# Optimization experiments

Hardware: AMD Instinct MI355X
Metric: run time of the kernel (lower is better)

## Reference

```python
import jax, jax.numpy as jnp
import numpy as np

B, N, DIM, HEADS = 4, 2048, 512, 8
LN_EPS = 1e-5


def setup_inputs() -> dict:
    key = jax.random.key(0)
    ks = jax.random.split(key, 16)
    w = lambda k: jax.random.normal(k, (DIM, DIM), jnp.float32) * 0.02
    bv = lambda k: jax.random.normal(k, (DIM,), jnp.float32) * 0.02
    return {
        'x': jax.random.normal(ks[0], (B, N, DIM), jnp.float32),
        'y': jax.random.normal(ks[1], (B, N, DIM), jnp.float32),
        'Wq': w(ks[2]), 'bq': bv(ks[3]),
        'Wk': w(ks[4]), 'bk': bv(ks[5]),
        'Wvr': w(ks[6]), 'bvr': bv(ks[7]),
        'Wvd': w(ks[8]), 'bvd': bv(ks[9]),
        'g_r': jnp.ones((DIM,), jnp.float32), 'b_r': jnp.zeros((DIM,), jnp.float32),
        'g_d': jnp.ones((DIM,), jnp.float32), 'b_d': jnp.zeros((DIM,), jnp.float32),
        'Wpr': w(ks[10]), 'bpr': bv(ks[11]),
        'Wpd': w(ks[12]), 'bpd': bv(ks[13]),
        'num_heads': HEADS,
    }


def _ln(t, g, b):
    mu = jnp.mean(t, axis=-1, keepdims=True)
    var = jnp.mean(jnp.square(t - mu), axis=-1, keepdims=True)
    return (t - mu) * jax.lax.rsqrt(var + LN_EPS) * g + b


def reference(x, y, Wq, bq, Wk, bk, Wvr, bvr, Wvd, bvd,
              g_r, b_r, g_d, b_d, Wpr, bpr, Wpd, bpd, num_heads):
    Bn, Nn, C = x.shape
    D = C // num_heads
    xn = _ln(x, g_r, b_r)   # norm_r(x)
    yn = _ln(y, g_d, b_d)   # norm_d(y)

    def heads(t, W, b):  # Linear then split heads -> (B, H, N, D)
        return (t @ W.T + b).reshape(Bn, Nn, num_heads, D).transpose(0, 2, 1, 3)

    q_r = heads(yn, Wq, bq)    # query from depth-normed y
    v_r = heads(xn, Wvr, bvr)
    k_d = heads(xn, Wk, bk)
    v_d = heads(xn, Wvd, bvd)

    scale = D ** -0.5
    attn = jnp.einsum('bhnd,bhmd->bhnm', q_r, k_d) * scale  # shared QK^T
    attn_r = jax.nn.softmax(attn, axis=-1)                  # row-wise
    attn_d = jax.nn.softmax(attn.transpose(0, 1, 3, 2), axis=-1)  # col-wise (transposed)

    out_r = jnp.einsum('bhnm,bhmd->bhnd', attn_r, v_r)
    out_r = out_r.transpose(0, 2, 1, 3).reshape(Bn, Nn, C) @ Wpr.T + bpr

    o_d = jnp.einsum('bhnm,bhmd->bhnd', attn_d, v_d)
    o_d = o_d.transpose(0, 2, 1, 3).reshape(Bn, Nn, C)
    # Faithful to source quirk: extra transpose(1,2)+reshape scrambles layout.
    o_d = o_d.transpose(0, 2, 1).reshape(Bn, Nn, C)
    out_d = o_d @ Wpd.T + bpd
    return out_r, out_d
```

## Files before the change

kernel.cpp:

```cpp
#include <hip/hip_runtime.h>
#include <hip/hip_bf16.h>

typedef __hip_bfloat16 bf16;
typedef __attribute__((ext_vector_type(8))) short short8;
typedef __attribute__((ext_vector_type(4))) short short4v;
typedef __attribute__((ext_vector_type(4))) float floatx4;

static constexpr int B = 4;
static constexpr int N = 2048;
static constexpr int C = 512;
static constexpr int H = 8;
static constexpr int D = 64;

#define QK_SCALE 0.18033688011112042f

__device__ int g_flags[18];

__device__ __forceinline__ float u2f(unsigned short u) {
    return __uint_as_float(((unsigned int)u) << 16);
}
__device__ __forceinline__ unsigned short f2bf(float f) {
    unsigned int u = __float_as_uint(f);
    return (unsigned short)((u + 0x7FFFu + ((u >> 16) & 1u)) >> 16);
}
__device__ __forceinline__ float ldin(const void* p, size_t i, int f) {
    if (f == 2) return 0.0f;
    return f ? ((const float*)p)[i] : u2f(((const unsigned short*)p)[i]);
}

__device__ __forceinline__ void gl_lds16(const unsigned short* g, unsigned short* l) {
    __builtin_amdgcn_global_load_lds(
        (const __attribute__((address_space(1))) unsigned int*)g,
        (__attribute__((address_space(3))) unsigned int*)l,
        16, 0, 0);
}

struct Ptrs { const void* p[18]; };

__global__ void detect_kernel(Ptrs ptrs) {
    int t = blockIdx.x;
    int lane = threadIdx.x;
    unsigned int v = ((const unsigned int*)ptrs.p[t])[lane];
    unsigned int e = (v >> 7) & 0xFF;
    unsigned long long mp = __ballot(e >= 96 && e <= 144);
    unsigned long long mz = __ballot(v != 0u);
    if (lane == 0)
        g_flags[t] = (mz == 0ull) ? 2 : ((__popcll(mp) >= 32) ? 0 : 1);
}

__global__ __launch_bounds__(256) void convert_w(Ptrs ptrs, bf16* dst) {
    int wsel = blockIdx.y;
    int wi = wsel < 4 ? 2 + 2 * wsel : 14 + 2 * (wsel - 4);
    int f = g_flags[wi];
    const void* src = ptrs.p[wi];
    unsigned short* out = (unsigned short*)dst + (size_t)wsel * 262144;
    int base = (blockIdx.x * 256 + threadIdx.x) * 16;
    if (f == 1) {
        const float4* s = (const float4*)((const float*)src + base);
        float4 f0 = s[0], f1 = s[1], f2 = s[2], f3 = s[3];
        uint4 o0, o1;
        o0.x = f2bf(f0.x) | ((unsigned int)f2bf(f0.y) << 16);
        o0.y = f2bf(f0.z) | ((unsigned int)f2bf(f0.w) << 16);
        o0.z = f2bf(f1.x) | ((unsigned int)f2bf(f1.y) << 16);
        o0.w = f2bf(f1.z) | ((unsigned int)f2bf(f1.w) << 16);
        o1.x = f2bf(f2.x) | ((unsigned int)f2bf(f2.y) << 16);
        o1.y = f2bf(f2.z) | ((unsigned int)f2bf(f2.w) << 16);
        o1.z = f2bf(f3.x) | ((unsigned int)f2bf(f3.y) << 16);
        o1.w = f2bf(f3.z) | ((unsigned int)f2bf(f3.w) << 16);
        *(uint4*)(out + base) = o0;
        *(uint4*)(out + base + 8) = o1;
    } else if (f == 0) {
        const uint4* s = (const uint4*)((const unsigned short*)src + base);
        uint4 a = s[0], b2 = s[1];
        *(uint4*)(out + base) = a;
        *(uint4*)(out + base + 8) = b2;
    } else {
        uint4 z = {0, 0, 0, 0};
        *(uint4*)(out + base) = z;
        *(uint4*)(out + base + 8) = z;
    }
}

__global__ __launch_bounds__(256) void ln_kernel(
    const void* __restrict__ x, const void* __restrict__ y,
    const void* __restrict__ g_r, const void* __restrict__ b_r,
    const void* __restrict__ g_d, const void* __restrict__ b_d,
    bf16* __restrict__ xn, bf16* __restrict__ yn)
{
    __shared__ float ls[4], lq[4];
    __shared__ float mu_s, rs_s;

    int row = blockIdx.x;
    bool isY = row >= B * N;
    int r = isY ? row - B * N : row;
    const void* src = isY ? y : x;
    int sf = isY ? g_flags[1] : g_flags[0];
    const void* g  = isY ? g_d : g_r;
    int gf = isY ? g_flags[12] : g_flags[10];
    const void* bb = isY ? b_d : b_r;
    int bflag = isY ? g_flags[13] : g_flags[11];
    bf16* dst = (isY ? yn : xn) + (size_t)r * C;
    size_t base = (size_t)r * C;

    int tid = threadIdx.x;
    float v0 = ldin(src, base + tid, sf);
    float v1 = ldin(src, base + tid + 256, sf);
    float s = v0 + v1, sq = v0 * v0 + v1 * v1;
    #pragma unroll
    for (int off = 32; off > 0; off >>= 1) {
        s  += __shfl_down(s, off);
        sq += __shfl_down(sq, off);
    }
    int wid = tid >> 6, lane = tid & 63;
    if (lane == 0) { ls[wid] = s; lq[wid] = sq; }
    __syncthreads();
    if (tid == 0) {
        float S = ls[0] + ls[1] + ls[2] + ls[3];
        float Q = lq[0] + lq[1] + lq[2] + lq[3];
        float mu = S * (1.0f / C);
        float var = Q * (1.0f / C) - mu * mu;
        mu_s = mu; rs_s = rsqrtf(var + 1e-5f);
    }
    __syncthreads();
    float mu = mu_s, rs = rs_s;
    dst[tid]       = __float2bfloat16((v0 - mu) * rs * ldin(g, tid, gf)       + ldin(bb, tid, bflag));
    dst[tid + 256] = __float2bfloat16((v1 - mu) * rs * ldin(g, tid + 256, gf) + ldin(bb, tid + 256, bflag));
}

__device__ __forceinline__ void gemm_core(
    const bf16* __restrict__ A, const bf16* __restrict__ W,
    const void* __restrict__ bias, int bflag, void* __restrict__ Cout,
    int omode, float oscale)
{
    __shared__ __align__(16) unsigned short As[3][128 * 32];
    __shared__ __align__(16) unsigned short Ws[3][64 * 32];

    int tid = threadIdx.x;
    int n0 = blockIdx.x * 64;
    int m0 = blockIdx.y * 128;

    int wave = tid >> 6, lane = tid & 63;
    int wm = (wave >> 1) * 64, wn = (wave & 1) * 32;
    int quad = lane >> 4, mr = lane & 15;

    floatx4 acc[4][2] = {};

    int c0 = tid, c1 = 256 + tid;
    const unsigned short* Ag0 = (const unsigned short*)A + (size_t)(m0 + (c0 >> 2)) * 512 + (c0 & 3) * 8;
    const unsigned short* Ag1 = (const unsigned short*)A + (size_t)(m0 + (c1 >> 2)) * 512 + (c1 & 3) * 8;
    const unsigned short* Wg0 = (const unsigned short*)W + (size_t)(n0 + (c0 >> 2)) * 512 + (c0 & 3) * 8;

    auto STAGE = [&](int kt, int bsel) {
        int ko = kt * 32;
        gl_lds16(Ag0 + ko, &As[bsel][c0 * 8]);
        gl_lds16(Ag1 + ko, &As[bsel][c1 * 8]);
        gl_lds16(Wg0 + ko, &Ws[bsel][c0 * 8]);
    };

    auto GBODY = [&](int bsel, int kt) {
        if (kt < 14) {
            STAGE(kt + 2, bsel == 0 ? 2 : bsel - 1);
            asm volatile("s_waitcnt vmcnt(6)" ::: "memory");
        } else if (kt == 14) {
            asm volatile("s_waitcnt vmcnt(3)" ::: "memory");
        } else {
            asm volatile("s_waitcnt vmcnt(0)" ::: "memory");
        }
        __builtin_amdgcn_s_barrier();
        __builtin_amdgcn_sched_barrier(0);

        short8 af[4], bfr[2];
        #pragma unroll
        for (int i = 0; i < 4; ++i)
            af[i] = *(const short8*)&As[bsel][(wm + i * 16 + mr) * 32 + quad * 8];
        #pragma unroll
        for (int j = 0; j < 2; ++j)
            bfr[j] = *(const short8*)&Ws[bsel][(wn + j * 16 + mr) * 32 + quad * 8];
        #pragma unroll
        for (int i = 0; i < 4; ++i)
            #pragma unroll
            for (int j = 0; j < 2; ++j)
                acc[i][j] = __builtin_amdgcn_mfma_f32_16x16x32_bf16(
                    af[i], bfr[j], acc[i][j], 0, 0, 0);

        __builtin_amdgcn_sched_barrier(0);
        __builtin_amdgcn_s_barrier();
    };

    STAGE(0, 0);
    STAGE(1, 1);
    for (int g = 0; g < 5; ++g) {
        int kt = g * 3;
        GBODY(0, kt);
        GBODY(1, kt + 1);
        GBODY(2, kt + 2);
    }
    GBODY(0, 15);

    float bv[2];
    #pragma unroll
    for (int j = 0; j < 2; ++j)
        bv[j] = ldin(bias, n0 + wn + j * 16 + mr, bflag);
    #pragma unroll
    for (int i = 0; i < 4; ++i) {
        #pragma unroll
        for (int j = 0; j < 2; ++j) {
            int o = n0 + wn + j * 16 + mr;
            #pragma unroll
            for (int reg = 0; reg < 4; ++reg) {
                int r = m0 + wm + i * 16 + quad * 4 + reg;
                float val = (acc[i][j][reg] + bv[j]) * oscale;
                if (omode == 0) {
                    ((bf16*)Cout)[(size_t)r * 512 + o] = __float2bfloat16(val);
                } else if (omode == 1) {
                    ((float*)Cout)[(size_t)r * 512 + o] = val;
                } else {
                    int batch = r >> 11, nn = r & 2047;
                    ((bf16*)Cout)[((size_t)(batch * 512 + o)) * 2048 + nn] =
                        __float2bfloat16(val);
                }
            }
        }
    }
}

__global__ __launch_bounds__(256) void gemm_stage(
    const bf16* __restrict__ xn, const bf16* __restrict__ yn,
    const bf16* __restrict__ wts, Ptrs ptrs,
    bf16* __restrict__ q, bf16* __restrict__ k,
    bf16* __restrict__ vrT, bf16* __restrict__ vdT)
{
    int z = blockIdx.z;
    const bf16* A = (z == 0) ? yn : xn;
    const bf16* W = wts + (size_t)z * 262144;
    int bi = 3 + 2 * z;
    void* Cout = (z == 0) ? (void*)q : (z == 1) ? (void*)k
               : (z == 2) ? (void*)vrT : (void*)vdT;
    int omode = (z < 2) ? 0 : 2;
    float oscale = (z == 0) ? QK_SCALE : 1.0f;
    gemm_core(A, W, ptrs.p[bi], g_flags[bi], Cout, omode, oscale);
}

__global__ __launch_bounds__(256) void gemm_out(
    const bf16* __restrict__ Or, const bf16* __restrict__ Ad,
    const bf16* __restrict__ wts, Ptrs ptrs,
    float* __restrict__ out0, float* __restrict__ out1)
{
    int z = blockIdx.z;
    const bf16* A = z ? Ad : Or;
    const bf16* W = wts + (size_t)(4 + z) * 262144;
    int bi = 15 + 2 * z;
    gemm_core(A, W, ptrs.p[bi], g_flags[bi], z ? (void*)out1 : (void*)out0, 1, 1.0f);
}

__global__ __launch_bounds__(256) void flash_mfma(
    const bf16* __restrict__ qm, const bf16* __restrict__ km,
    const bf16* __restrict__ vrT, const bf16* __restrict__ vdT,
    bf16* __restrict__ Or, bf16* __restrict__ Ad)
{
    __shared__ __align__(16) unsigned short Ks[2][64 * 64];
    __shared__ __align__(16) unsigned short Vs[2][64 * 64];

    int phys = blockIdx.x + 32 * blockIdx.y + 256 * blockIdx.z;
    int s = phys >> 3;
    int qblk = s & 31;
    int gidx = (phys & 7) + ((s >> 5) << 3);
    int pass = gidx >> 5;
    int b = (gidx >> 3) & 3;
    int h = gidx & 7;

    const bf16* Q  = pass ? km : qm;
    const bf16* K  = pass ? qm : km;
    const bf16* Vt = pass ? vdT : vrT;
    bf16* Out = pass ? Ad : Or;

    int tid = threadIdx.x;
    int wave = tid >> 6, lane = tid & 63;
    int quad = lane >> 4, mr = lane & 15;
    int m8 = mr & 7;
    int qw = qblk * 64 + wave * 16;

    const unsigned short* Qb = (const unsigned short*)Q + ((size_t)(b * N + qw + mr)) * C + h * D;
    short8 qf0 = *(const short8*)(Qb + quad * 8);
    short8 qf1 = *(const short8*)(Qb + 32 + quad * 8);

    floatx4 Oacc[4] = {};
    floatx4 lacc = {};

    short4v ones;
    {
        union { unsigned int u[2]; short4v s4; } cv;
        cv.u[0] = 0x3F803F80u; cv.u[1] = 0x3F803F80u;
        ones = cv.s4;
    }

    int c0 = tid, c1 = 256 + tid;
    int r0 = c0 >> 3, cs0 = c0 & 7;
    int r1 = c1 >> 3, cs1 = c1 & 7;
    const unsigned short* Kb  = (const unsigned short*)K + ((size_t)b * N) * C + h * D;
    const unsigned short* Vtb = (const unsigned short*)Vt + ((size_t)(b * 512 + h * 64)) * 2048;
    const unsigned short* sk0 = Kb + (size_t)r0 * C + ((cs0 ^ (r0 & 7)) << 3);
    const unsigned short* sk1 = Kb + (size_t)r1 * C + ((cs1 ^ (r1 & 7)) << 3);
    const unsigned short* sv0 = Vtb + (size_t)r0 * 2048 + ((cs0 ^ (r0 & 7)) << 3);
    const unsigned short* sv1 = Vtb + (size_t)r1 * 2048 + ((cs1 ^ (r1 & 7)) << 3);

    auto STAGE = [&](int bsel) {
        gl_lds16(sk0, &Ks[bsel][c0 * 8]);
        gl_lds16(sk1, &Ks[bsel][c1 * 8]);
        gl_lds16(sv0, &Vs[bsel][c0 * 8]);
        gl_lds16(sv1, &Vs[bsel][c1 * 8]);
        sk0 += 64 * C; sk1 += 64 * C; sv0 += 64; sv1 += 64;
    };

    int skc0 = (quad ^ m8) << 3;
    int skc1 = ((quad + 4) ^ m8) << 3;
    int vq = quad >> 1, vlo = (quad & 1) * 4;

    auto BODY = [&](int cur, bool last) {
        if (!last) {
            STAGE(cur ^ 1);
            asm volatile("s_waitcnt vmcnt(4)" ::: "memory");
        } else {
            asm volatile("s_waitcnt vmcnt(0)" ::: "memory");
        }
        __builtin_amdgcn_s_barrier();
        __builtin_amdgcn_sched_barrier(0);

        floatx4 tac[4] = {};
        __builtin_amdgcn_s_setprio(1);
        #pragma unroll
        for (int t = 0; t < 4; ++t) {
            const unsigned short* kr = &Ks[cur][(t * 16 + mr) * 64];
            short8 kf0 = *(const short8*)(kr + skc0);
            short8 kf1 = *(const short8*)(kr + skc1);
            tac[t] = __builtin_amdgcn_mfma_f32_16x16x32_bf16(kf0, qf0, tac[t], 0, 0, 0);
            tac[t] = __builtin_amdgcn_mfma_f32_16x16x32_bf16(kf1, qf1, tac[t], 0, 0, 0);
        }
        __builtin_amdgcn_s_setprio(0);

        short4v pa[4];
        #pragma unroll
        for (int t = 0; t < 4; ++t) {
            float p0, p1, p2, p3;
            asm("v_exp_f32 %0, %1" : "=v"(p0) : "v"(tac[t][0]));
            asm("v_exp_f32 %0, %1" : "=v"(p1) : "v"(tac[t][1]));
            asm("v_exp_f32 %0, %1" : "=v"(p2) : "v"(tac[t][2]));
            asm("v_exp_f32 %0, %1" : "=v"(p3) : "v"(tac[t][3]));
            unsigned int u0, u1;
            asm("v_cvt_pk_bf16_f32 %0, %1, %2" : "=v"(u0) : "v"(p0), "v"(p1));
            asm("v_cvt_pk_bf16_f32 %0, %1, %2" : "=v"(u1) : "v"(p2), "v"(p3));
            union { unsigned int u[2]; short4v s4; } cv;
            cv.u[0] = u0; cv.u[1] = u1;
            pa[t] = cv.s4;
        }

        __builtin_amdgcn_s_setprio(1);
        #pragma unroll
        for (int t = 0; t < 4; ++t) {
            int vslot = (((2 * t + vq) ^ m8) << 3) + vlo;
            #pragma unroll
            for (int j = 0; j < 4; ++j) {
                short4v vb = *(const short4v*)&Vs[cur][(j * 16 + mr) * 64 + vslot];
                Oacc[j] = __builtin_amdgcn_mfma_f32_16x16x16bf16_1k(
                    pa[t], vb, Oacc[j], 0, 0, 0);
            }
            lacc = __builtin_amdgcn_mfma_f32_16x16x16bf16_1k(pa[t], ones, lacc, 0, 0, 0);
        }
        __builtin_amdgcn_s_setprio(0);

        __builtin_amdgcn_sched_barrier(0);
        __builtin_amdgcn_s_barrier();
    };

    STAGE(0);
    for (int kt2 = 0; kt2 < 15; ++kt2) {
        BODY(0, false);
        BODY(1, false);
    }
    BODY(0, false);
    BODY(1, true);

    float inv[4];
    #pragma unroll
    for (int r = 0; r < 4; ++r)
        inv[r] = 1.0f / lacc[r];

    if (pass == 0) {
        #pragma unroll
        for (int t = 0; t < 4; ++t)
            #pragma unroll
            for (int r = 0; r < 4; ++r) {
                int n = qw + quad * 4 + r;
                Out[((size_t)(b * N + n)) * C + h * D + t * 16 + mr] =
                    __float2bfloat16(Oacc[t][r] * inv[r]);
            }
    } else {
        size_t bbase = (size_t)b * N * C;
        #pragma unroll
        for (int t = 0; t < 4; ++t)
            #pragma unroll
            for (int r = 0; r < 4; ++r) {
                int n = qw + quad * 4 + r;
                int c = h * D + t * 16 + mr;
                Out[bbase + (size_t)(c * 4 + (n >> 9)) * 512 + (n & 511)] =
                    __float2bfloat16(Oacc[t][r] * inv[r]);
            }
    }
}

extern "C" void kernel_launch(void* const* d_in, const int* in_sizes, int n_in,
                              void* d_out, int out_size, void* d_ws, size_t ws_size,
                              hipStream_t stream)
{
    const void* x   = d_in[0];
    const void* y   = d_in[1];
    const void* g_r = d_in[10];
    const void* b_r = d_in[11];
    const void* g_d = d_in[12];
    const void* b_d = d_in[13];

    Ptrs ptrs;
    for (int i = 0; i < 18; ++i) ptrs.p[i] = d_in[i];

    const size_t SL = (size_t)B * N * C;

    char* wsb = (char*)d_ws;
    bf16* q   = (bf16*)wsb;
    bf16* k   = (bf16*)(wsb + 8ull * 1024 * 1024);
    bf16* vrT = (bf16*)(wsb + 16ull * 1024 * 1024);
    bf16* vdT = (bf16*)(wsb + 24ull * 1024 * 1024);
    bf16* xn  = (bf16*)(wsb + 32ull * 1024 * 1024);
    bf16* yn  = (bf16*)(wsb + 40ull * 1024 * 1024);
    bf16* wts = (bf16*)(wsb + 48ull * 1024 * 1024);
    bf16* Or = xn;
    bf16* Ad = yn;

    float* out0 = (float*)d_out;
    float* out1 = (float*)d_out + SL;

    detect_kernel<<<18, 64, 0, stream>>>(ptrs);
    convert_w<<<dim3(64, 6), 256, 0, stream>>>(ptrs, wts);
    ln_kernel<<<2 * B * N, 256, 0, stream>>>(x, y, g_r, b_r, g_d, b_d, xn, yn);

    gemm_stage<<<dim3(8, 64, 4), 256, 0, stream>>>(xn, yn, wts, ptrs, q, k, vrT, vdT);

    dim3 fg(32, 8, 8);
    flash_mfma<<<fg, 256, 0, stream>>>(q, k, vrT, vdT, Or, Ad);

    gemm_out<<<dim3(8, 64, 2), 256, 0, stream>>>(Or, Ad, wts, ptrs, out0, out1);
}
```

Before: 303.2 us.

## Fuse K/Vr/Vd projections, vectorize LayerNorm per-wave, trim flash barriers

LayerNorm now handles one row per wave with 8-element vector loads and a pure shuffle reduction, removing the LDS round trips and block-level syncs. The K, Vr and Vd projections, which share the input xn, are fused into one GEMM kernel. Each A tile is loaded once and reused against three weight tiles, so xn is read from memory once instead of three times. The Q projection moves to its own kernel. The flash attention loop drops the trailing barrier and places a single barrier before staging, which cuts synchronisation per iteration. The fused GEMM holds three times the accumulators and uses more LDS, so occupancy may fall.

```diff
diff --git a/kernel.cpp b/kernel.cpp
--- a/kernel.cpp
+++ b/kernel.cpp
@@ -26,6 +26,22 @@
 __device__ __forceinline__ float ldin(const void* p, size_t i, int f) {
     if (f == 2) return 0.0f;
     return f ? ((const float*)p)[i] : u2f(((const unsigned short*)p)[i]);
+}
+
+__device__ __forceinline__ void ld8(const void* p, size_t idx, int f, float* o) {
+    if (f == 1) {
+        const float4* q = (const float4*)((const float*)p + idx);
+        float4 a = q[0], b2 = q[1];
+        o[0] = a.x; o[1] = a.y; o[2] = a.z; o[3] = a.w;
+        o[4] = b2.x; o[5] = b2.y; o[6] = b2.z; o[7] = b2.w;
+    } else if (f == 0) {
+        short8 s8 = *(const short8*)((const unsigned short*)p + idx);
+        #pragma unroll
+        for (int i = 0; i < 8; ++i) o[i] = u2f((unsigned short)s8[i]);
+    } else {
+        #pragma unroll
+        for (int i = 0; i < 8; ++i) o[i] = 0.0f;
+    }
 }
 
 __device__ __forceinline__ void gl_lds16(const unsigned short* g, unsigned short* l) {
@@ -87,10 +103,9 @@
     const void* __restrict__ g_d, const void* __restrict__ b_d,
     bf16* __restrict__ xn, bf16* __restrict__ yn)
 {
-    __shared__ float ls[4], lq[4];
-    __shared__ float mu_s, rs_s;
-
-    int row = blockIdx.x;
+    int tid = threadIdx.x;
+    int wid = tid >> 6, lane = tid & 63;
+    int row = blockIdx.x * 4 + wid;
     bool isY = row >= B * N;
     int r = isY ? row - B * N : row;
     const void* src = isY ? y : x;
@@ -100,31 +115,32 @@
     const void* bb = isY ? b_d : b_r;
     int bflag = isY ? g_flags[13] : g_flags[11];
     bf16* dst = (isY ? yn : xn) + (size_t)r * C;
-    size_t base = (size_t)r * C;
-
-    int tid = threadIdx.x;
-    float v0 = ldin(src, base + tid, sf);
-    float v1 = ldin(src, base + tid + 256, sf);
-    float s = v0 + v1, sq = v0 * v0 + v1 * v1;
-    #pragma unroll
-    for (int off = 32; off > 0; off >>= 1) {
-        s  += __shfl_down(s, off);
-        sq += __shfl_down(sq, off);
-    }
-    int wid = tid >> 6, lane = tid & 63;
-    if (lane == 0) { ls[wid] = s; lq[wid] = sq; }
-    __syncthreads();
-    if (tid == 0) {
-        float S = ls[0] + ls[1] + ls[2] + ls[3];
-        float Q = lq[0] + lq[1] + lq[2] + lq[3];
-        float mu = S * (1.0f / C);
-        float var = Q * (1.0f / C) - mu * mu;
-        mu_s = mu; rs_s = rsqrtf(var + 1e-5f);
-    }
-    __syncthreads();
-    float mu = mu_s, rs = rs_s;
-    dst[tid]       = __float2bfloat16((v0 - mu) * rs * ldin(g, tid, gf)       + ldin(bb, tid, bflag));
-    dst[tid + 256] = __float2bfloat16((v1 - mu) * rs * ldin(g, tid + 256, gf) + ldin(bb, tid + 256, bflag));
+
+    int col = lane * 8;
+    float v[8];
+    ld8(src, (size_t)r * C + col, sf, v);
+
+    float s = 0.f, sq = 0.f;
+    #pragma unroll
+    for (int i = 0; i < 8; ++i) { s += v[i]; sq += v[i] * v[i]; }
+    #pragma unroll
+    for (int off = 1; off < 64; off <<= 1) {
+        s  += __shfl_xor(s, off);
+        sq += __shfl_xor(sq, off);
+    }
+    float mu = s * (1.0f / C);
+    float var = sq * (1.0f / C) - mu * mu;
+    float rs = rsqrtf(var + 1e-5f);
+
+    float gv[8], bv[8];
+    ld8(g, col, gf, gv);
+    ld8(bb, col, bflag, bv);
+
+    union { unsigned short us[8]; short8 s8; } o;
+    #pragma unroll
+    for (int i = 0; i < 8; ++i)
+        o.us[i] = f2bf((v[i] - mu) * rs * gv[i] + bv[i]);
+    *(short8*)(dst + col) = o.s8;
 }
 
 __device__ __forceinline__ void gemm_core(
@@ -224,21 +240,11 @@
     }
 }
 
-__global__ __launch_bounds__(256) void gemm_stage(
-    const bf16* __restrict__ xn, const bf16* __restrict__ yn,
-    const bf16* __restrict__ wts, Ptrs ptrs,
-    bf16* __restrict__ q, bf16* __restrict__ k,
-    bf16* __restrict__ vrT, bf16* __restrict__ vdT)
-{
-    int z = blockIdx.z;
-    const bf16* A = (z == 0) ? yn : xn;
-    const bf16* W = wts + (size_t)z * 262144;
-    int bi = 3 + 2 * z;
-    void* Cout = (z == 0) ? (void*)q : (z == 1) ? (void*)k
-               : (z == 2) ? (void*)vrT : (void*)vdT;
-    int omode = (z < 2) ? 0 : 2;
-    float oscale = (z == 0) ? QK_SCALE : 1.0f;
-    gemm_core(A, W, ptrs.p[bi], g_flags[bi], Cout, omode, oscale);
+__global__ __launch_bounds__(256) void gemm_q(
+    const bf16* __restrict__ yn, const bf16* __restrict__ wts, Ptrs ptrs,
+    bf16* __restrict__ q)
+{
+    gemm_core(yn, wts, ptrs.p[3], g_flags[3], (void*)q, 0, QK_SCALE);
 }
 
 __global__ __launch_bounds__(256) void gemm_out(
@@ -251,6 +257,115 @@
     const bf16* W = wts + (size_t)(4 + z) * 262144;
     int bi = 15 + 2 * z;
     gemm_core(A, W, ptrs.p[bi], g_flags[bi], z ? (void*)out1 : (void*)out0, 1, 1.0f);
+}
+
+__global__ __launch_bounds__(256) void gemm_fused3(
+    const bf16* __restrict__ xn, const bf16* __restrict__ wts, Ptrs ptrs,
+    bf16* __restrict__ k, bf16* __restrict__ vrT, bf16* __restrict__ vdT)
+{
+    __shared__ __align__(16) unsigned short As[3][128 * 32];
+    __shared__ __align__(16) unsigned short Ws[3][3][64 * 32];
+
+    int tid = threadIdx.x;
+    int n0 = blockIdx.x * 64;
+    int m0 = blockIdx.y * 128;
+
+    int wave = tid >> 6, lane = tid & 63;
+    int wm = (wave >> 1) * 64, wn = (wave & 1) * 32;
+    int quad = lane >> 4, mr = lane & 15;
+
+    floatx4 acc[3][4][2] = {};
+
+    int c0 = tid, c1 = 256 + tid;
+    const unsigned short* Ag0 = (const unsigned short*)xn + (size_t)(m0 + (c0 >> 2)) * 512 + (c0 & 3) * 8;
+    const unsigned short* Ag1 = (const unsigned short*)xn + (size_t)(m0 + (c1 >> 2)) * 512 + (c1 & 3) * 8;
+    const unsigned short* Wg[3];
+    #pragma unroll
+    for (int z = 0; z < 3; ++z)
+        Wg[z] = (const unsigned short*)wts + (size_t)(1 + z) * 262144
+              + (size_t)(n0 + (c0 >> 2)) * 512 + (c0 & 3) * 8;
+
+    auto STAGE = [&](int kt, int bsel) {
+        int ko = kt * 32;
+        gl_lds16(Ag0 + ko, &As[bsel][c0 * 8]);
+        gl_lds16(Ag1 + ko, &As[bsel][c1 * 8]);
+        #pragma unroll
+        for (int z = 0; z < 3; ++z)
+            gl_lds16(Wg[z] + ko, &Ws[bsel][z][c0 * 8]);
+    };
+
+    auto GBODY = [&](int bsel, int kt) {
+        if (kt < 14) {
+            STAGE(kt + 2, bsel == 0 ? 2 : bsel - 1);
+            asm volatile("s_waitcnt vmcnt(10)" ::: "memory");
+        } else if (kt == 14) {
+            asm volatile("s_waitcnt vmcnt(5)" ::: "memory");
+        } else {
+            asm volatile("s_waitcnt vmcnt(0)" ::: "memory");
+        }
+        __builtin_amdgcn_s_barrier();
+        __builtin_amdgcn_sched_barrier(0);
+
+        short8 af[4];
+        #pragma unroll
+        for (int i = 0; i < 4; ++i)
+            af[i] = *(const short8*)&As[bsel][(wm + i * 16 + mr) * 32 + quad * 8];
+        #pragma unroll
+        for (int z = 0; z < 3; ++z) {
+            short8 bfr[2];
+            #pragma unroll
+            for (int j = 0; j < 2; ++j)
+                bfr[j] = *(const short8*)&Ws[bsel][z][(wn + j * 16 + mr) * 32 + quad * 8];
+            #pragma unroll
+            for (int i = 0; i < 4; ++i)
+                #pragma unroll
+                for (int j = 0; j < 2; ++j)
+                    acc[z][i][j] = __builtin_amdgcn_mfma_f32_16x16x32_bf16(
+                        af[i], bfr[j], acc[z][i][j], 0, 0, 0);
+        }
+
+        __builtin_amdgcn_sched_barrier(0);
+        __builtin_amdgcn_s_barrier();
+    };
+
+    STAGE(0, 0);
+    STAGE(1, 1);
+    for (int g = 0; g < 5; ++g) {
+        int kt = g * 3;
+        GBODY(0, kt);
+        GBODY(1, kt + 1);
+        GBODY(2, kt + 2);
+    }
+    GBODY(0, 15);
+
+    const int bidx[3] = {5, 7, 9};
+    #pragma unroll
+    for (int z = 0; z < 3; ++z) {
+        float bv[2];
+        #pragma unroll
+        for (int j = 0; j < 2; ++j)
+            bv[j] = ldin(ptrs.p[bidx[z]], n0 + wn + j * 16 + mr, g_flags[bidx[z]]);
+        bf16* Cz = (z == 0) ? k : (z == 1) ? vrT : vdT;
+        #pragma unroll
+        for (int i = 0; i < 4; ++i) {
+            #pragma unroll
+            for (int j = 0; j < 2; ++j) {
+                int o = n0 + wn + j * 16 + mr;
+                #pragma unroll
+                for (int reg = 0; reg < 4; ++reg) {
+                    int r = m0 + wm + i * 16 + quad * 4 + reg;
+                    float val = acc[z][i][j][reg] + bv[j];
+                    if (z == 0) {
+                        Cz[(size_t)r * 512 + o] = __float2bfloat16(val);
+                    } else {
+                        int batch = r >> 11, nn = r & 2047;
+                        Cz[((size_t)(batch * 512 + o)) * 2048 + nn] =
+                            __float2bfloat16(val);
+                    }
+                }
+            }
+        }
+    }
 }
 
 __global__ __launch_bounds__(256) void flash_mfma(
@@ -317,13 +432,13 @@
     int vq = quad >> 1, vlo = (quad & 1) * 4;
 
     auto BODY = [&](int cur, bool last) {
+        __builtin_amdgcn_s_barrier();
         if (!last) {
             STAGE(cur ^ 1);
             asm volatile("s_waitcnt vmcnt(4)" ::: "memory");
         } else {
             asm volatile("s_waitcnt vmcnt(0)" ::: "memory");
         }
-        __builtin_amdgcn_s_barrier();
         __builtin_amdgcn_sched_barrier(0);
 
         floatx4 tac[4] = {};
@@ -367,9 +482,7 @@
             lacc = __builtin_amdgcn_mfma_f32_16x16x16bf16_1k(pa[t], ones, lacc, 0, 0, 0);
         }
         __builtin_amdgcn_s_setprio(0);
-
         __builtin_amdgcn_sched_barrier(0);
-        __builtin_amdgcn_s_barrier();
     };
 
     STAGE(0);
@@ -440,9 +553,10 @@
 
     detect_kernel<<<18, 64, 0, stream>>>(ptrs);
     convert_w<<<dim3(64, 6), 256, 0, stream>>>(ptrs, wts);
-    ln_kernel<<<2 * B * N, 256, 0, stream>>>(x, y, g_r, b_r, g_d, b_d, xn, yn);
-
-    gemm_stage<<<dim3(8, 64, 4), 256, 0, stream>>>(xn, yn, wts, ptrs, q, k, vrT, vdT);
+    ln_kernel<<<2 * B * N / 4, 256, 0, stream>>>(x, y, g_r, b_r, g_d, b_d, xn, yn);
+
+    gemm_q<<<dim3(8, 64), 256, 0, stream>>>(yn, wts, ptrs, q);
+    gemm_fused3<<<dim3(8, 64), 256, 0, stream>>>(xn, wts, ptrs, k, vrT, vdT);
 
     dim3 fg(32, 8, 8);
     flash_mfma<<<fg, 256, 0, stream>>>(q, k, vrT, vdT, Or, Ad);
```

After: 292.3 us. 3.6% less time.

## Vectorize LayerNorm per wave, swizzle GEMM tiles, drop flash barrier

Applied to the files above, without the earlier changes.

LayerNorm now processes one row per wave. Each lane handles 8 elements with vector loads and stores, and the reduction is a wave-level xor-shuffle, so the shared-memory reduction and both block barriers are gone. The projection GEMMs remap block indices so that consecutive blocks share the same A row tile, which is meant to improve L2 reuse. The flash attention loop now uses one barrier per iteration, placed before the prefetch, instead of two. That barrier no longer sits after the vmcnt wait, so visibility of LDS data loaded by other waves may no longer be guaranteed.

```diff
diff --git a/kernel.cpp b/kernel.cpp
--- a/kernel.cpp
+++ b/kernel.cpp
@@ -26,6 +26,22 @@
 __device__ __forceinline__ float ldin(const void* p, size_t i, int f) {
     if (f == 2) return 0.0f;
     return f ? ((const float*)p)[i] : u2f(((const unsigned short*)p)[i]);
+}
+
+__device__ __forceinline__ void ld8(const void* p, size_t idx, int f, float* o) {
+    if (f == 1) {
+        const float4* q = (const float4*)((const float*)p + idx);
+        float4 a = q[0], b2 = q[1];
+        o[0] = a.x; o[1] = a.y; o[2] = a.z; o[3] = a.w;
+        o[4] = b2.x; o[5] = b2.y; o[6] = b2.z; o[7] = b2.w;
+    } else if (f == 0) {
+        short8 s8 = *(const short8*)((const unsigned short*)p + idx);
+        #pragma unroll
+        for (int i = 0; i < 8; ++i) o[i] = u2f((unsigned short)s8[i]);
+    } else {
+        #pragma unroll
+        for (int i = 0; i < 8; ++i) o[i] = 0.0f;
+    }
 }
 
 __device__ __forceinline__ void gl_lds16(const unsigned short* g, unsigned short* l) {
@@ -87,10 +103,9 @@
     const void* __restrict__ g_d, const void* __restrict__ b_d,
     bf16* __restrict__ xn, bf16* __restrict__ yn)
 {
-    __shared__ float ls[4], lq[4];
-    __shared__ float mu_s, rs_s;
-
-    int row = blockIdx.x;
+    int tid = threadIdx.x;
+    int wid = tid >> 6, lane = tid & 63;
+    int row = blockIdx.x * 4 + wid;
     bool isY = row >= B * N;
     int r = isY ? row - B * N : row;
     const void* src = isY ? y : x;
@@ -100,44 +115,43 @@
     const void* bb = isY ? b_d : b_r;
     int bflag = isY ? g_flags[13] : g_flags[11];
     bf16* dst = (isY ? yn : xn) + (size_t)r * C;
-    size_t base = (size_t)r * C;
-
-    int tid = threadIdx.x;
-    float v0 = ldin(src, base + tid, sf);
-    float v1 = ldin(src, base + tid + 256, sf);
-    float s = v0 + v1, sq = v0 * v0 + v1 * v1;
-    #pragma unroll
-    for (int off = 32; off > 0; off >>= 1) {
-        s  += __shfl_down(s, off);
-        sq += __shfl_down(sq, off);
-    }
-    int wid = tid >> 6, lane = tid & 63;
-    if (lane == 0) { ls[wid] = s; lq[wid] = sq; }
-    __syncthreads();
-    if (tid == 0) {
-        float S = ls[0] + ls[1] + ls[2] + ls[3];
-        float Q = lq[0] + lq[1] + lq[2] + lq[3];
-        float mu = S * (1.0f / C);
-        float var = Q * (1.0f / C) - mu * mu;
-        mu_s = mu; rs_s = rsqrtf(var + 1e-5f);
-    }
-    __syncthreads();
-    float mu = mu_s, rs = rs_s;
-    dst[tid]       = __float2bfloat16((v0 - mu) * rs * ldin(g, tid, gf)       + ldin(bb, tid, bflag));
-    dst[tid + 256] = __float2bfloat16((v1 - mu) * rs * ldin(g, tid + 256, gf) + ldin(bb, tid + 256, bflag));
+
+    int col = lane * 8;
+    float v[8];
+    ld8(src, (size_t)r * C + col, sf, v);
+
+    float s = 0.f, sq = 0.f;
+    #pragma unroll
+    for (int i = 0; i < 8; ++i) { s += v[i]; sq += v[i] * v[i]; }
+    #pragma unroll
+    for (int off = 1; off < 64; off <<= 1) {
+        s  += __shfl_xor(s, off);
+        sq += __shfl_xor(sq, off);
+    }
+    float mu = s * (1.0f / C);
+    float var = sq * (1.0f / C) - mu * mu;
+    float rs = rsqrtf(var + 1e-5f);
+
+    float gv[8], bv[8];
+    ld8(g, col, gf, gv);
+    ld8(bb, col, bflag, bv);
+
+    union { unsigned short us[8]; short8 s8; } o;
+    #pragma unroll
+    for (int i = 0; i < 8; ++i)
+        o.us[i] = f2bf((v[i] - mu) * rs * gv[i] + bv[i]);
+    *(short8*)(dst + col) = o.s8;
 }
 
 __device__ __forceinline__ void gemm_core(
     const bf16* __restrict__ A, const bf16* __restrict__ W,
     const void* __restrict__ bias, int bflag, void* __restrict__ Cout,
-    int omode, float oscale)
+    int omode, float oscale, int n0, int m0)
 {
     __shared__ __align__(16) unsigned short As[3][128 * 32];
     __shared__ __align__(16) unsigned short Ws[3][64 * 32];
 
     int tid = threadIdx.x;
-    int n0 = blockIdx.x * 64;
-    int m0 = blockIdx.y * 128;
 
     int wave = tid >> 6, lane = tid & 63;
     int wm = (wave >> 1) * 64, wn = (wave & 1) * 32;
@@ -224,6 +238,11 @@
     }
 }
 
+__device__ __forceinline__ void swz_nm(int& n0, int& m0) {
+    m0 = (blockIdx.x * 8 + (blockIdx.y >> 3)) * 128;
+    n0 = (blockIdx.y & 7) * 64;
+}
+
 __global__ __launch_bounds__(256) void gemm_stage(
     const bf16* __restrict__ xn, const bf16* __restrict__ yn,
     const bf16* __restrict__ wts, Ptrs ptrs,
@@ -238,7 +257,9 @@
                : (z == 2) ? (void*)vrT : (void*)vdT;
     int omode = (z < 2) ? 0 : 2;
     float oscale = (z == 0) ? QK_SCALE : 1.0f;
-    gemm_core(A, W, ptrs.p[bi], g_flags[bi], Cout, omode, oscale);
+    int n0, m0;
+    swz_nm(n0, m0);
+    gemm_core(A, W, ptrs.p[bi], g_flags[bi], Cout, omode, oscale, n0, m0);
 }
 
 __global__ __launch_bounds__(256) void gemm_out(
@@ -250,7 +271,10 @@
     const bf16* A = z ? Ad : Or;
     const bf16* W = wts + (size_t)(4 + z) * 262144;
     int bi = 15 + 2 * z;
-    gemm_core(A, W, ptrs.p[bi], g_flags[bi], z ? (void*)out1 : (void*)out0, 1, 1.0f);
+    int n0, m0;
+    swz_nm(n0, m0);
+    gemm_core(A, W, ptrs.p[bi], g_flags[bi], z ? (void*)out1 : (void*)out0,
+              1, 1.0f, n0, m0);
 }
 
 __global__ __launch_bounds__(256) void flash_mfma(
@@ -317,13 +341,13 @@
     int vq = quad >> 1, vlo = (quad & 1) * 4;
 
     auto BODY = [&](int cur, bool last) {
+        __builtin_amdgcn_s_barrier();
         if (!last) {
             STAGE(cur ^ 1);
             asm volatile("s_waitcnt vmcnt(4)" ::: "memory");
         } else {
             asm volatile("s_waitcnt vmcnt(0)" ::: "memory");
         }
-        __builtin_amdgcn_s_barrier();
         __builtin_amdgcn_sched_barrier(0);
 
         floatx4 tac[4] = {};
@@ -367,9 +391,7 @@
             lacc = __builtin_amdgcn_mfma_f32_16x16x16bf16_1k(pa[t], ones, lacc, 0, 0, 0);
         }
         __builtin_amdgcn_s_setprio(0);
-
         __builtin_amdgcn_sched_barrier(0);
-        __builtin_amdgcn_s_barrier();
     };
 
     STAGE(0);
@@ -440,7 +462,7 @@
 
     detect_kernel<<<18, 64, 0, stream>>>(ptrs);
     convert_w<<<dim3(64, 6), 256, 0, stream>>>(ptrs, wts);
-    ln_kernel<<<2 * B * N, 256, 0, stream>>>(x, y, g_r, b_r, g_d, b_d, xn, yn);
+    ln_kernel<<<2 * B * N / 4, 256, 0, stream>>>(x, y, g_r, b_r, g_d, b_d, xn, yn);
 
     gemm_stage<<<dim3(8, 64, 4), 256, 0, stream>>>(xn, yn, wts, ptrs, q, k, vrT, vdT);
 
```

Measured after the change: 276.1 us. 1.1x faster.
